# Performance work log

Hardware: AMD Instinct MI355X
Metric: run time of the kernel (lower is better)

## Reference

```python
import jax, jax.numpy as jnp
import numpy as np


def _reflect(x, size):
    # PyTorch grid_sample reflection padding, align_corners=False:
    # reflect about borders at -0.5 and size-0.5, then clip to [0, size-1].
    x = x + 0.5
    x = jnp.mod(x, 2.0 * size)
    x = jnp.where(x >= size, 2.0 * size - x, x)
    x = x - 0.5
    return jnp.clip(x, 0.0, size - 1.0)


def _grid_sample_one(img, grid):
    # img: (H, W, C); grid: (H, W, 2) with (x, y) in [-1, 1]
    H, W, _ = img.shape
    # unnormalize, align_corners=False
    ix = ((grid[..., 0] + 1.0) * W - 1.0) * 0.5
    iy = ((grid[..., 1] + 1.0) * H - 1.0) * 0.5
    ix = _reflect(ix, W)
    iy = _reflect(iy, H)
    x0 = jnp.floor(ix)
    y0 = jnp.floor(iy)
    wx = (ix - x0)[..., None]
    wy = (iy - y0)[..., None]
    x0i = jnp.clip(x0, 0, W - 1).astype(jnp.int32)
    x1i = jnp.clip(x0 + 1.0, 0, W - 1).astype(jnp.int32)
    y0i = jnp.clip(y0, 0, H - 1).astype(jnp.int32)
    y1i = jnp.clip(y0 + 1.0, 0, H - 1).astype(jnp.int32)
    Ia = img[y0i, x0i]  # (H, W, C)
    Ib = img[y0i, x1i]
    Ic = img[y1i, x0i]
    Id = img[y1i, x1i]
    return (Ia * (1 - wx) * (1 - wy) + Ib * wx * (1 - wy)
            + Ic * (1 - wx) * wy + Id * wx * wy)


def _displace(image, displacement_map, amplitude, angle):
    N, H, W, C = image.shape
    # base sampling grid, torch.linspace(-1, 1, size) endpoints included
    gy, gx = jnp.meshgrid(jnp.linspace(-1.0, 1.0, H, dtype=image.dtype),
                          jnp.linspace(-1.0, 1.0, W, dtype=image.dtype),
                          indexing='ij')
    base = jnp.stack([gx, gy], axis=-1)  # (H, W, 2) as (x, y)
    # bilinear resize (half-pixel centers == torch align_corners=False)
    dm = jax.image.resize(displacement_map,
                          (N, H, W, displacement_map.shape[-1]),
                          method='bilinear')
    if dm.shape[-1] == 3:
        dm = jnp.mean(dm, axis=-1)  # (N, H, W)
    else:
        dm = dm[..., 0]
    d = dm * amplitude[:, None, None]
    dx = jnp.cos(angle)[:, None, None] * d / (W - 1) * 2.0
    dy = jnp.sin(angle)[:, None, None] * d / (H - 1) * 2.0
    grid = base[None] + jnp.stack([dx, dy], axis=-1)  # (N, H, W, 2)
    return jax.vmap(_grid_sample_one)(image, grid)  # (N, H, W, C)


def setup_inputs() -> dict:
    key = jax.random.key(0)
    k1, k2, k3, k4 = jax.random.split(key, 4)
    N, H, W, C = 8, 1024, 1024, 3
    image = jax.random.normal(k1, (N, H, W, C), dtype=jnp.float32)
    displacement_map = jax.random.uniform(k2, (N, 512, 512, 3), dtype=jnp.float32)
    amplitude = jax.random.uniform(k3, (N,), dtype=jnp.float32) * 20.0  # pixels
    angle = jax.random.uniform(k4, (N,), dtype=jnp.float32) * 2.0 * np.pi
    return {"image": image, "displacement_map": displacement_map,
            "amplitude": amplitude, "angle": angle}


def reference(image, displacement_map, amplitude, angle):
    return _displace(image, displacement_map, amplitude, angle)
```

## Files before the change

### kernel.cpp

```cpp
#include <hip/hip_runtime.h>
#include <math.h>

__global__ __launch_bounds__(256) void prep_kernel(
    const float* __restrict__ dmap, const float* __restrict__ amp,
    const float* __restrict__ ang, float* __restrict__ sc,
    float* __restrict__ rd, long long npix, int N, float fx, float fy) {
    long long p = (long long)blockIdx.x * 256 + threadIdx.x;
    if (p < npix) {
        const float* s = dmap + p * 3;
        rd[p] = s[0] + s[1] + s[2];
    }
    if (blockIdx.x == 0 && (int)threadIdx.x < N) {
        int i = threadIdx.x;
        float s_, c_;
        sincosf(ang[i], &s_, &c_);
        float a = amp[i] * (1.0f / 3.0f);
        sc[2 * i]     = c_ * a * fx;
        sc[2 * i + 1] = s_ * a * fy;
    }
}

__global__ __launch_bounds__(1024, 8) void displace_main(
    const float* __restrict__ img,
    const float* __restrict__ rd,
    const float* __restrict__ sc,
    float* __restrict__ out)
{
    const int lin = (int)blockIdx.y * 1024 + (int)blockIdx.x;
    const int hl  = (lin & 7) * 1024 + (lin >> 3);
    const int n   = hl >> 10;
    const int h   = hl & 1023;
    const int w   = threadIdx.x;

    const int dy0 = max((h - 1) >> 1, 0);
    const int dy1 = min((h + 1) >> 1, 511);
    const float ty = (h & 1) ? 0.25f : 0.75f;
    const float* r0 = rd + (n * 512 + dy0) * 512;
    const float* r1 = rd + (n * 512 + dy1) * 512;
    const float scx = sc[2 * n];
    const float scy = sc[2 * n + 1];
    const float* ibase = img + (long long)n * (1024 * 1024 * 3);

    const int dx0 = max((w - 1) >> 1, 0);
    const int dx1 = min((w + 1) >> 1, 511);
    const float tx = (w & 1) ? 0.25f : 0.75f;
    float a0 = r0[dx0], b0 = r0[dx1];
    float a1 = r1[dx0], b1 = r1[dx1];
    float m0 = fmaf(b0 - a0, tx, a0);
    float m1 = fmaf(b1 - a1, tx, a1);
    float ds = fmaf(m1 - m0, ty, m0);

    const float C = 1024.0f / 1023.0f;
    float ux = fmaf((float)w, C, ds * scx);
    float uy = fmaf((float)h, C, ds * scy);

    ux = fabsf(ux); if (ux >= 1024.0f) ux = 2048.0f - ux;
    uy = fabsf(uy); if (uy >= 1024.0f) uy = 2048.0f - uy;
    float ix = fminf(fmaxf(ux - 0.5f, 0.0f), 1023.0f);
    float iy = fminf(fmaxf(uy - 0.5f, 0.0f), 1023.0f);

    int ix0 = (int)ix;
    int iy0 = (int)iy;
    float wx = ix - (float)ix0;
    float wy = iy - (float)iy0;
    int ix1 = min(ix0 + 1, 1023);
    int iy1 = min(iy0 + 1, 1023);

    const float* Ia = ibase + ((iy0 << 10) + ix0) * 3;
    const float* Ib = ibase + ((iy0 << 10) + ix1) * 3;
    const float* Ic = ibase + ((iy1 << 10) + ix0) * 3;
    const float* Id = ibase + ((iy1 << 10) + ix1) * 3;

    const float wa = (1.0f - wx) * (1.0f - wy);
    const float wb = wx * (1.0f - wy);
    const float wc = (1.0f - wx) * wy;
    const float wd = wx * wy;

    float* o = out + ((hl << 10) + w) * 3;
    o[0] = Ia[0] * wa + Ib[0] * wb + Ic[0] * wc + Id[0] * wd;
    o[1] = Ia[1] * wa + Ib[1] * wb + Ic[1] * wc + Id[1] * wd;
    o[2] = Ia[2] * wa + Ib[2] * wb + Ic[2] * wc + Id[2] * wd;
}

__device__ __forceinline__ float reflect_dyn(float x, float size) {
    x += 0.5f;
    float two = 2.0f * size;
    x = x - floorf(x / two) * two;
    if (x >= size) x = two - x;
    x -= 0.5f;
    return fminf(fmaxf(x, 0.0f), size - 1.0f);
}

__global__ __launch_bounds__(256) void displace_fallback(
    const float* __restrict__ img, const float* __restrict__ dmap,
    const float* __restrict__ amp, const float* __restrict__ ang,
    float* __restrict__ out, int N, int H, int W, int DH, int DW)
{
    long long idx = (long long)blockIdx.x * blockDim.x + threadIdx.x;
    long long total = (long long)N * H * W;
    if (idx >= total) return;
    int w = (int)(idx % W);
    long long t = idx / W;
    int h = (int)(t % H);
    int n = (int)(t / H);

    float sx = (w + 0.5f) * ((float)DW / (float)W) - 0.5f;
    float sy = (h + 0.5f) * ((float)DH / (float)H) - 0.5f;
    float fx = floorf(sx), fy = floorf(sy);
    float tx = sx - fx, ty = sy - fy;
    int dx0 = max(0, min(DW - 1, (int)fx));
    int dx1 = max(0, min(DW - 1, (int)fx + 1));
    int dy0 = max(0, min(DH - 1, (int)fy));
    int dy1 = max(0, min(DH - 1, (int)fy + 1));
    const float* dbase = dmap + (long long)n * DH * DW * 3;
    const float* p00 = dbase + ((long long)dy0 * DW + dx0) * 3;
    const float* p01 = dbase + ((long long)dy0 * DW + dx1) * 3;
    const float* p10 = dbase + ((long long)dy1 * DW + dx0) * 3;
    const float* p11 = dbase + ((long long)dy1 * DW + dx1) * 3;
    float m00 = p00[0] + p00[1] + p00[2];
    float m01 = p01[0] + p01[1] + p01[2];
    float m10 = p10[0] + p10[1] + p10[2];
    float m11 = p11[0] + p11[1] + p11[2];
    float dmv = ((m00 * (1.0f - tx) + m01 * tx) * (1.0f - ty)
               + (m10 * (1.0f - tx) + m11 * tx) * ty) * (1.0f / 3.0f);
    float a = amp[n], an = ang[n], sa, ca;
    sincosf(an, &sa, &ca);
    float d = dmv * a;
    float gx = -1.0f + 2.0f * (float)w / (float)(W - 1) + ca * d * (2.0f / (float)(W - 1));
    float gy = -1.0f + 2.0f * (float)h / (float)(H - 1) + sa * d * (2.0f / (float)(H - 1));
    float ixf2 = ((gx + 1.0f) * (float)W - 1.0f) * 0.5f;
    float iyf2 = ((gy + 1.0f) * (float)H - 1.0f) * 0.5f;
    ixf2 = reflect_dyn(ixf2, (float)W);
    iyf2 = reflect_dyn(iyf2, (float)H);
    float x0f = floorf(ixf2), y0f = floorf(iyf2);
    float wx = ixf2 - x0f, wy = iyf2 - y0f;
    int ix0 = min((int)x0f, W - 1);
    int ix1 = min((int)x0f + 1, W - 1);
    int iy0 = min((int)y0f, H - 1);
    int iy1 = min((int)y0f + 1, H - 1);
    const float* ibase = img + (long long)n * H * W * 3;
    const float* Ia = ibase + ((long long)iy0 * W + ix0) * 3;
    const float* Ib = ibase + ((long long)iy0 * W + ix1) * 3;
    const float* Ic = ibase + ((long long)iy1 * W + ix0) * 3;
    const float* Id = ibase + ((long long)iy1 * W + ix1) * 3;
    float wa = (1.0f - wx) * (1.0f - wy);
    float wb = wx * (1.0f - wy);
    float wc = (1.0f - wx) * wy;
    float wd = wx * wy;
    float* o = out + idx * 3;
    #pragma unroll
    for (int c = 0; c < 3; ++c)
        o[c] = Ia[c] * wa + Ib[c] * wb + Ic[c] * wc + Id[c] * wd;
}

extern "C" void kernel_launch(void* const* d_in, const int* in_sizes, int n_in,
                              void* d_out, int out_size, void* d_ws, size_t ws_size,
                              hipStream_t stream) {
    const float* img  = (const float*)d_in[0];
    const float* dmap = (const float*)d_in[1];
    const float* amp  = (const float*)d_in[2];
    const float* ang  = (const float*)d_in[3];
    float* out = (float*)d_out;

    int N = in_sizes[2];
    long long hw  = (long long)in_sizes[0] / ((long long)N * 3);
    int H = (int)llround(sqrt((double)hw));
    int W = H;
    long long dhw = (long long)in_sizes[1] / ((long long)N * 3);
    int DH = (int)llround(sqrt((double)dhw));
    int DW = DH;

    size_t need = 256 + (size_t)N * DH * DW * sizeof(float);

    if (H == 1024 && W == 1024 && DH == 512 && DW == 512 && N <= 256 &&
        ws_size >= need) {
        float* sc = (float*)d_ws;
        float* rd = (float*)((char*)d_ws + 256);

        long long npix = (long long)N * DH * DW;
        int pgrid = (int)((npix + 255) / 256);
        prep_kernel<<<pgrid, 256, 0, stream>>>(
            dmap, amp, ang, sc, rd, npix, N,
            (float)W / (float)(W - 1), (float)H / (float)(H - 1));

        dim3 grid(1024, (unsigned)N);
        displace_main<<<grid, 1024, 0, stream>>>(img, rd, sc, out);
    } else {
        long long total = (long long)N * H * W;
        int block = 256;
        long long grid = (total + block - 1) / block;
        displace_fallback<<<(dim3)(unsigned)grid, block, 0, stream>>>(
            img, dmap, amp, ang, out, N, H, W, DH, DW);
    }
}
```

Measured before the change: 242.8 us.

## Retile displace kernel to 256-thread blocks covering four rows each

The main kernel now uses 256-thread blocks, each handling a quarter-row segment across four consecutive output rows. The block index interleaves batches so neighbouring blocks work on different images, as before. Each thread loops over the four rows, reusing its per-column setup (horizontal displacement indices and weights, base x coordinate) and giving more memory-level parallelism per thread. The fast path is restricted to N == 8 because the grid size is now hard-coded, which narrows when the specialised kernel is used.

```diff
diff --git a/kernel.cpp b/kernel.cpp
--- a/kernel.cpp
+++ b/kernel.cpp
@@ -20,66 +20,74 @@
     }
 }
 
-__global__ __launch_bounds__(1024, 8) void displace_main(
+__global__ __launch_bounds__(256) void displace_main(
     const float* __restrict__ img,
     const float* __restrict__ rd,
     const float* __restrict__ sc,
     float* __restrict__ out)
 {
-    const int lin = (int)blockIdx.y * 1024 + (int)blockIdx.x;
-    const int hl  = (lin & 7) * 1024 + (lin >> 3);
-    const int n   = hl >> 10;
-    const int h   = hl & 1023;
-    const int w   = threadIdx.x;
-
-    const int dy0 = max((h - 1) >> 1, 0);
-    const int dy1 = min((h + 1) >> 1, 511);
-    const float ty = (h & 1) ? 0.25f : 0.75f;
-    const float* r0 = rd + (n * 512 + dy0) * 512;
-    const float* r1 = rd + (n * 512 + dy1) * 512;
+    const int lin  = (int)blockIdx.x;
+    const int n    = lin & 7;
+    const int rest = lin >> 3;
+    const int h0   = (rest >> 2) << 2;
+    const int w    = ((rest & 3) << 8) + (int)threadIdx.x;
+
     const float scx = sc[2 * n];
     const float scy = sc[2 * n + 1];
     const float* ibase = img + (long long)n * (1024 * 1024 * 3);
+    const float* rbase = rd + n * (512 * 512);
 
     const int dx0 = max((w - 1) >> 1, 0);
     const int dx1 = min((w + 1) >> 1, 511);
     const float tx = (w & 1) ? 0.25f : 0.75f;
-    float a0 = r0[dx0], b0 = r0[dx1];
-    float a1 = r1[dx0], b1 = r1[dx1];
-    float m0 = fmaf(b0 - a0, tx, a0);
-    float m1 = fmaf(b1 - a1, tx, a1);
-    float ds = fmaf(m1 - m0, ty, m0);
-
     const float C = 1024.0f / 1023.0f;
-    float ux = fmaf((float)w, C, ds * scx);
-    float uy = fmaf((float)h, C, ds * scy);
-
-    ux = fabsf(ux); if (ux >= 1024.0f) ux = 2048.0f - ux;
-    uy = fabsf(uy); if (uy >= 1024.0f) uy = 2048.0f - uy;
-    float ix = fminf(fmaxf(ux - 0.5f, 0.0f), 1023.0f);
-    float iy = fminf(fmaxf(uy - 0.5f, 0.0f), 1023.0f);
-
-    int ix0 = (int)ix;
-    int iy0 = (int)iy;
-    float wx = ix - (float)ix0;
-    float wy = iy - (float)iy0;
-    int ix1 = min(ix0 + 1, 1023);
-    int iy1 = min(iy0 + 1, 1023);
-
-    const float* Ia = ibase + ((iy0 << 10) + ix0) * 3;
-    const float* Ib = ibase + ((iy0 << 10) + ix1) * 3;
-    const float* Ic = ibase + ((iy1 << 10) + ix0) * 3;
-    const float* Id = ibase + ((iy1 << 10) + ix1) * 3;
-
-    const float wa = (1.0f - wx) * (1.0f - wy);
-    const float wb = wx * (1.0f - wy);
-    const float wc = (1.0f - wx) * wy;
-    const float wd = wx * wy;
-
-    float* o = out + ((hl << 10) + w) * 3;
-    o[0] = Ia[0] * wa + Ib[0] * wb + Ic[0] * wc + Id[0] * wd;
-    o[1] = Ia[1] * wa + Ib[1] * wb + Ic[1] * wc + Id[1] * wd;
-    o[2] = Ia[2] * wa + Ib[2] * wb + Ic[2] * wc + Id[2] * wd;
+    const float uxb = (float)w * C;
+
+    #pragma unroll
+    for (int k = 0; k < 4; ++k) {
+        const int h = h0 + k;
+        const int dy0 = max((h - 1) >> 1, 0);
+        const int dy1 = min((h + 1) >> 1, 511);
+        const float ty = (h & 1) ? 0.25f : 0.75f;
+        const float* r0 = rbase + (dy0 << 9);
+        const float* r1 = rbase + (dy1 << 9);
+
+        float a0 = r0[dx0], b0 = r0[dx1];
+        float a1 = r1[dx0], b1 = r1[dx1];
+        float m0 = fmaf(b0 - a0, tx, a0);
+        float m1 = fmaf(b1 - a1, tx, a1);
+        float ds = fmaf(m1 - m0, ty, m0);
+
+        float ux = fmaf(ds, scx, uxb);
+        float uy = fmaf(ds, scy, (float)h * C);
+
+        ux = fabsf(ux); if (ux >= 1024.0f) ux = 2048.0f - ux;
+        uy = fabsf(uy); if (uy >= 1024.0f) uy = 2048.0f - uy;
+        float ix = fminf(fmaxf(ux - 0.5f, 0.0f), 1023.0f);
+        float iy = fminf(fmaxf(uy - 0.5f, 0.0f), 1023.0f);
+
+        int ix0 = (int)ix;
+        int iy0 = (int)iy;
+        float wx = ix - (float)ix0;
+        float wy = iy - (float)iy0;
+        int ix1 = min(ix0 + 1, 1023);
+        int iy1 = min(iy0 + 1, 1023);
+
+        const float* Ia = ibase + ((iy0 << 10) + ix0) * 3;
+        const float* Ib = ibase + ((iy0 << 10) + ix1) * 3;
+        const float* Ic = ibase + ((iy1 << 10) + ix0) * 3;
+        const float* Id = ibase + ((iy1 << 10) + ix1) * 3;
+
+        const float wa = (1.0f - wx) * (1.0f - wy);
+        const float wb = wx * (1.0f - wy);
+        const float wc = (1.0f - wx) * wy;
+        const float wd = wx * wy;
+
+        float* o = out + (((long long)(n << 10 | h) << 10) + w) * 3;
+        o[0] = Ia[0] * wa + Ib[0] * wb + Ic[0] * wc + Id[0] * wd;
+        o[1] = Ia[1] * wa + Ib[1] * wb + Ic[1] * wc + Id[1] * wd;
+        o[2] = Ia[2] * wa + Ib[2] * wb + Ic[2] * wc + Id[2] * wd;
+    }
 }
 
 __device__ __forceinline__ float reflect_dyn(float x, float size) {
@@ -172,7 +180,7 @@
 
     size_t need = 256 + (size_t)N * DH * DW * sizeof(float);
 
-    if (H == 1024 && W == 1024 && DH == 512 && DW == 512 && N <= 256 &&
+    if (H == 1024 && W == 1024 && DH == 512 && DW == 512 && N == 8 &&
         ws_size >= need) {
         float* sc = (float*)d_ws;
         float* rd = (float*)((char*)d_ws + 256);
@@ -183,8 +191,7 @@
             dmap, amp, ang, sc, rd, npix, N,
             (float)W / (float)(W - 1), (float)H / (float)(H - 1));
 
-        dim3 grid(1024, (unsigned)N);
-        displace_main<<<grid, 1024, 0, stream>>>(img, rd, sc, out);
+        displace_main<<<8192, 256, 0, stream>>>(img, rd, sc, out);
     } else {
         long long total = (long long)N * H * W;
         int block = 256;
```

Result: faster. 232.3 us (-4.3%).
